# Performance work log

Hardware: AMD Instinct MI355X
Metric: run time of the kernel (lower is better)

Reference implementation:

```python
import jax, jax.numpy as jnp
import numpy as np

BN_EPS = 1e-3  # keras BatchNormalization default epsilon
NEG_INF = -1e30


def _masked_row_softmax(adjT):
    # tf.sparse.softmax semantics: softmax over NONZERO entries of each row;
    # implicit zeros stay exactly zero.
    mask = adjT != 0
    logits = jnp.where(mask, adjT, NEG_INF)
    p = jax.nn.softmax(logits, axis=-1)
    return jnp.where(mask, p, 0.0)


def _batch_norm(x, gamma, beta):
    # training-mode BN over all axes except channels
    mean = jnp.mean(x, axis=(0, 1), keepdims=True)
    var = jnp.var(x, axis=(0, 1), keepdims=True)
    return (x - mean) * jax.lax.rsqrt(var + BN_EPS) * gamma + beta


def setup_inputs() -> dict:
    key = jax.random.key(0)
    ks = jax.random.split(key, 4)
    B, N, F = 1, 8192, 128
    C0, C1 = 256, 128
    features = jax.random.normal(ks[0], (B, N, F), dtype=jnp.float32)
    adj = jax.random.randint(ks[1], (B, N, N), 0, 2, dtype=jnp.int32)
    kernel_1 = jax.random.normal(ks[2], (F, C0), dtype=jnp.float32) * (1.0 / np.sqrt(F))
    kernel_2 = jax.random.normal(ks[3], (C0, C1), dtype=jnp.float32) * (1.0 / np.sqrt(C0))
    return {
        "features": features,
        "adj": adj,
        "kernel_1": kernel_1,
        "bias_1": jnp.zeros((C0,), jnp.float32),
        "gamma_1": jnp.ones((C0,), jnp.float32),
        "beta_1": jnp.zeros((C0,), jnp.float32),
        "kernel_2": kernel_2,
        "bias_2": jnp.zeros((C1,), jnp.float32),
        "gamma_2": jnp.ones((C1,), jnp.float32),
        "beta_2": jnp.zeros((C1,), jnp.float32),
    }


def reference(features, adj, kernel_1, bias_1, gamma_1, beta_1,
              kernel_2, bias_2, gamma_2, beta_2):
    # fltr transposed: (B, Nr, Np), then sparse softmax over last dim
    adjT = jnp.transpose(adj.astype(jnp.float32), (0, 2, 1))
    w = _masked_row_softmax(adjT)                      # (B, Nr, Np)
    # people -> region aggregation + projection
    region = jnp.matmul(w, features)                   # (B, Nr, F)
    region = jnp.matmul(region, kernel_1) + bias_1     # (B, Nr, C0)
    region = _batch_norm(region, gamma_1, beta_1)
    # region -> people aggregation + projection
    people = jnp.matmul(jnp.transpose(w, (0, 2, 1)), region)  # (B, Np, C0)
    people = jnp.matmul(people, kernel_2) + bias_2             # (B, Np, C1)
    people = _batch_norm(people, gamma_2, beta_2)
    return people
```

## Files before the change

### kernel.cpp

```cpp
#include <hip/hip_runtime.h>
#include <stdint.h>

typedef unsigned int u32;
typedef unsigned short u16;
typedef unsigned long long u64;
typedef __attribute__((ext_vector_type(8))) short short8;
typedef __attribute__((ext_vector_type(4))) float f32x4;

#define N8K 8192

__device__ __forceinline__ float b2f(u16 u) { return __uint_as_float(((u32)u) << 16); }
__device__ __forceinline__ u16 f2b(float f) {
  u32 i = __float_as_uint(f);
  i += 0x7FFFu + ((i >> 16) & 1u);
  return (u16)(i >> 16);
}
__device__ __forceinline__ u16 f2h(float f) {
  union { _Float16 h; u16 u; } x; x.h = (_Float16)f; return x.u;
}
__device__ __forceinline__ u32 pkh(float a, float b) {
  return (u32)f2h(a) | ((u32)f2h(b) << 16);
}
union H8 { uint4 u; _Float16 h[8]; };
union H2 { u32 u; _Float16 h[2]; };
__device__ __forceinline__ u32 pk01(int x, int y) { return (u32)__mul24(x | (y << 16), 0x3F80); }
__device__ __forceinline__ u32 pkf(float a, float b) { return (u32)f2b(a) | ((u32)f2b(b) << 16); }

__device__ __forceinline__ int dvote(const u16* f16) {
  u16 u = f16[threadIdx.x * 2];
  int e = (u >> 7) & 0xFF;
  return __syncthreads_count((e >= 0x60 && e <= 0x9F) ? 1 : 0) >= 128;
}

__device__ __forceinline__ void gl_lds16(const void* g, void* l) {
  __builtin_amdgcn_global_load_lds(
      (const __attribute__((address_space(1))) u32*)g,
      (__attribute__((address_space(3))) u32*)l, 16, 0, 0);
}

__device__ __forceinline__ void unpack16(u32 b, uint4& o0, uint4& o1) {
  o0.x = ((b & 0x0001u) ? 0x3F80u : 0u) | ((b & 0x0002u) ? 0x3F800000u : 0u);
  o0.y = ((b & 0x0004u) ? 0x3F80u : 0u) | ((b & 0x0008u) ? 0x3F800000u : 0u);
  o0.z = ((b & 0x0010u) ? 0x3F80u : 0u) | ((b & 0x0020u) ? 0x3F800000u : 0u);
  o0.w = ((b & 0x0040u) ? 0x3F80u : 0u) | ((b & 0x0080u) ? 0x3F800000u : 0u);
  o1.x = ((b & 0x0100u) ? 0x3F80u : 0u) | ((b & 0x0200u) ? 0x3F800000u : 0u);
  o1.y = ((b & 0x0400u) ? 0x3F80u : 0u) | ((b & 0x0800u) ? 0x3F800000u : 0u);
  o1.z = ((b & 0x1000u) ? 0x3F80u : 0u) | ((b & 0x2000u) ? 0x3F800000u : 0u);
  o1.w = ((b & 0x4000u) ? 0x3F80u : 0u) | ((b & 0x8000u) ? 0x3F800000u : 0u);
}

#define MFMA_4x4(As_, Bs_, aoff_, boff_)                                         \
  {                                                                              \
    short8 afr[4], bfr[4];                                                       \
    _Pragma("unroll") for (int i_ = 0; i_ < 4; ++i_)                             \
      afr[i_] = *(const short8*)(As_ + aoff_[i_]);                               \
    _Pragma("unroll") for (int j_ = 0; j_ < 4; ++j_)                             \
      bfr[j_] = *(const short8*)(Bs_ + boff_[j_]);                               \
    _Pragma("unroll") for (int i_ = 0; i_ < 4; ++i_)                             \
      _Pragma("unroll") for (int j_ = 0; j_ < 4; ++j_)                           \
        acc[i_][j_] = __builtin_amdgcn_mfma_f32_16x16x32_bf16(                   \
            afr[i_], bfr[j_], acc[i_][j_], 0, 0, 0);                             \
  }

#define ZERO_ACC()                                                               \
  f32x4 acc[4][4];                                                               \
  {                                                                              \
    const f32x4 fz = {0.f, 0.f, 0.f, 0.f};                                       \
    _Pragma("unroll") for (int i_ = 0; i_ < 4; ++i_)                             \
      _Pragma("unroll") for (int j_ = 0; j_ < 4; ++j_) acc[i_][j_] = fz;         \
  }

__global__ void k_prep(const void* __restrict__ featv, const void* __restrict__ K1v,
                       const void* __restrict__ K2v,
                       const void* __restrict__ b1v, const void* __restrict__ g1v,
                       const void* __restrict__ be1v, const void* __restrict__ b2v,
                       const void* __restrict__ g2v, const void* __restrict__ be2v,
                       u16* __restrict__ Ft, u16* __restrict__ K1T, u16* __restrict__ K2T,
                       float* __restrict__ deg, float* __restrict__ par,
                       float* __restrict__ bn1s, float* __restrict__ bn1q,
                       float* __restrict__ bn2s, float* __restrict__ bn2q) {
  const int b = blockIdx.x, t = threadIdx.x;
  const int flag = dvote((const u16*)featv);
  if (b < 256) {
    __shared__ __align__(16) u16 Lf[32 * 136];
    const int pr = t >> 3, ck = t & 7;
    u16 v[16];
    if (flag) {
      const u16* s = (const u16*)featv + (size_t)(b * 32 + pr) * 128 + ck * 16;
      *(uint4*)&v[0] = *(const uint4*)(s);
      *(uint4*)&v[8] = *(const uint4*)(s + 8);
    } else {
      const float* s = (const float*)featv + (size_t)(b * 32 + pr) * 128 + ck * 16;
#pragma unroll
      for (int i = 0; i < 16; ++i) v[i] = f2b(s[i]);
    }
    *(uint4*)(Lf + pr * 136 + ck * 16) = *(uint4*)&v[0];
    *(uint4*)(Lf + pr * 136 + ck * 16 + 8) = *(uint4*)&v[8];
    __syncthreads();
    const int f = t >> 1, h16 = (t & 1) * 16;
    u32 w[8];
#pragma unroll
    for (int i = 0; i < 8; ++i) {
      u16 lo = Lf[(h16 + 2 * i) * 136 + f];
      u16 hi = Lf[(h16 + 2 * i + 1) * 136 + f];
      w[i] = (u32)lo | ((u32)hi << 16);
    }
    u16* d = Ft + (size_t)b * 4096 + f * 32 + h16;
    *(uint4*)(d) = *(uint4*)&w[0];
    *(uint4*)(d + 8) = *(uint4*)&w[4];
  } else if (b < 272) {
    int o = ((b - 256) * 256 + t) << 3;
    int k0 = o >> 13, c = (o >> 5) & 255, kk = o & 31;
    uint4 w;
    if (flag) {
      const u16* s = (const u16*)K1v + (size_t)(k0 * 32 + kk) * 256 + c;
      w.x = (u32)s[0]    | ((u32)s[256]  << 16);
      w.y = (u32)s[512]  | ((u32)s[768]  << 16);
      w.z = (u32)s[1024] | ((u32)s[1280] << 16);
      w.w = (u32)s[1536] | ((u32)s[1792] << 16);
    } else {
      const float* s = (const float*)K1v + (size_t)(k0 * 32 + kk) * 256 + c;
      w.x = pkf(s[0], s[256]); w.y = pkf(s[512], s[768]);
      w.z = pkf(s[1024], s[1280]); w.w = pkf(s[1536], s[1792]);
    }
    *(uint4*)(K1T + o) = w;
  } else if (b < 288) {
    int o = ((b - 272) * 256 + t) << 3;
    int k0 = o >> 12, c = (o >> 5) & 127, kk = o & 31;
    uint4 w;
    if (flag) {
      const u16* s = (const u16*)K2v + (size_t)(k0 * 32 + kk) * 128 + c;
      w.x = (u32)s[0]   | ((u32)s[128] << 16);
      w.y = (u32)s[256] | ((u32)s[384] << 16);
      w.z = (u32)s[512] | ((u32)s[640] << 16);
      w.w = (u32)s[768] | ((u32)s[896] << 16);
    } else {
      const float* s = (const float*)K2v + (size_t)(k0 * 32 + kk) * 128 + c;
      w.x = pkf(s[0], s[128]); w.y = pkf(s[256], s[384]);
      w.z = pkf(s[512], s[640]); w.w = pkf(s[768], s[896]);
    }
    *(uint4*)(K2T + o) = w;
  } else {
    if (t < 256) {
      par[t]       = flag ? b2f(((const u16*)b1v)[t])  : ((const float*)b1v)[t];
      par[256 + t] = flag ? b2f(((const u16*)g1v)[t])  : ((const float*)g1v)[t];
      par[512 + t] = flag ? b2f(((const u16*)be1v)[t]) : ((const float*)be1v)[t];
      bn1s[t] = 0.f; bn1q[t] = 0.f;
    }
    if (t < 128) {
      par[768 + t]  = flag ? b2f(((const u16*)b2v)[t])  : ((const float*)b2v)[t];
      par[896 + t]  = flag ? b2f(((const u16*)g2v)[t])  : ((const float*)g2v)[t];
      par[1024 + t] = flag ? b2f(((const u16*)be2v)[t]) : ((const float*)be2v)[t];
      bn2s[t] = 0.f; bn2q[t] = 0.f;
    }
    for (int i = t; i < N8K; i += 256) deg[i] = 0.f;
  }
}

__global__ __launch_bounds__(256, 2)
void k_gemm1(const int* __restrict__ adj, const u16* __restrict__ Ft,
             u16* __restrict__ P1h, float* __restrict__ deg,
             u32* __restrict__ RB) {
  __shared__ __align__(16) u16 As[4 * 128 * 32];
  __shared__ __align__(16) u16 Bs[4 * 128 * 32];
  __shared__ float degp[128];
  const int t = threadIdx.x, bx = blockIdx.x;
  const int nt = bx & 63, s = bx >> 6;
  const int n0 = nt << 7;
  const int lane = t & 63, wv = t >> 6;
  const int wm = (wv & 1) << 6, wn = (wv >> 1) << 6;
  const int fm = lane & 15, fq = lane >> 4;
  if (t < 128) degp[t] = 0.0f;
  ZERO_ACC();
  int aoff[4], boff[4];
#pragma unroll
  for (int i = 0; i < 4; ++i) aoff[i] = (wm + i * 16 + fm) * 32 + fq * 8;
#pragma unroll
  for (int j = 0; j < 4; ++j) {
    int n = wn + j * 16 + fm;
    boff[j] = n * 32 + ((fq * 8) ^ (((n >> 2) & 3) << 3));
  }
  const int rb = t & 31, kb = t >> 5;
  const int* gB = adj + ((size_t)s * 1024 + kb * 4) * N8K + n0 + rb * 4;
  const char* gA = (const char*)(Ft + (size_t)s * 32 * 4096);
  char* lA = (char*)As + ((t >> 6) << 10);
  const int goff = t << 4;
  u16* lb0 = Bs + (rb * 4) * 32 + ((kb * 4) ^ ((rb & 3) << 3));
  const int sh4 = (rb & 7) * 4;
  const int rbw = (n0 >> 5) + (rb >> 3);
  const int pb0 = s * 1024 + kb * 4;
  int ds0 = 0, ds1 = 0, ds2 = 0, ds3 = 0;
  for (int ks = 0; ks < 8; ++ks) {
    __syncthreads();
#pragma unroll
    for (int ph = 0; ph < 8; ++ph) gl_lds16(gA + ph * 4096 + goff, lA + ph * 4096);
    gA += 32768;
    u32* dst = RB + (size_t)(pb0 + ks * 128) * 256 + rbw;
#pragma unroll
    for (int ph = 0; ph < 4; ++ph) {
      const int* g = gB + (size_t)ph * 32 * N8K;
      int4 a0 = *(const int4*)(g);
      int4 a1 = *(const int4*)(g + N8K);
      int4 a2 = *(const int4*)(g + 2 * N8K);
      int4 a3 = *(const int4*)(g + 3 * N8K);
      ds0 += a0.x + a1.x + a2.x + a3.x;
      ds1 += a0.y + a1.y + a2.y + a3.y;
      ds2 += a0.z + a1.z + a2.z + a3.z;
      ds3 += a0.w + a1.w + a2.w + a3.w;
      u16* lb = lb0 + ph * 4096;
      uint2 w;
      w.x = pk01(a0.x, a1.x); w.y = pk01(a2.x, a3.x); *(uint2*)(lb) = w;
      w.x = pk01(a0.y, a1.y); w.y = pk01(a2.y, a3.y); *(uint2*)(lb + 32) = w;
      w.x = pk01(a0.z, a1.z); w.y = pk01(a2.z, a3.z); *(uint2*)(lb + 64) = w;
      w.x = pk01(a0.w, a1.w); w.y = pk01(a2.w, a3.w); *(uint2*)(lb + 96) = w;
      u32 v0 = ((u32)a0.x | ((u32)a0.y << 1) | ((u32)a0.z << 2) | ((u32)a0.w << 3)) << sh4;
      u32 v1 = ((u32)a1.x | ((u32)a1.y << 1) | ((u32)a1.z << 2) | ((u32)a1.w << 3)) << sh4;
      u32 v2 = ((u32)a2.x | ((u32)a2.y << 1) | ((u32)a2.z << 2) | ((u32)a2.w << 3)) << sh4;
      u32 v3 = ((u32)a3.x | ((u32)a3.y << 1) | ((u32)a3.z << 2) | ((u32)a3.w << 3)) << sh4;
      v0 |= __shfl_xor(v0, 1); v0 |= __shfl_xor(v0, 2); v0 |= __shfl_xor(v0, 4);
      v1 |= __shfl_xor(v1, 1); v1 |= __shfl_xor(v1, 2); v1 |= __shfl_xor(v1, 4);
      v2 |= __shfl_xor(v2, 1); v2 |= __shfl_xor(v2, 2); v2 |= __shfl_xor(v2, 4);
      v3 |= __shfl_xor(v3, 1); v3 |= __shfl_xor(v3, 2); v3 |= __shfl_xor(v3, 4);
      if ((rb & 7) == 0) {
        u32* d2 = dst + ph * 8192;
        d2[0] = v0; d2[256] = v1; d2[512] = v2; d2[768] = v3;
      }
    }
    gB += 128 * N8K;
    __syncthreads();
#pragma unroll
    for (int ph = 0; ph < 4; ++ph)
      MFMA_4x4((As + ph * 4096), (Bs + ph * 4096), aoff, boff);
  }
  atomicAdd(&degp[rb * 4 + 0], (float)ds0);
  atomicAdd(&degp[rb * 4 + 1], (float)ds1);
  atomicAdd(&degp[rb * 4 + 2], (float)ds2);
  atomicAdd(&degp[rb * 4 + 3], (float)ds3);
  u16* base = P1h + ((size_t)s * N8K + n0) * 128;
#pragma unroll
  for (int i = 0; i < 4; ++i)
#pragma unroll
    for (int j = 0; j < 4; ++j) {
      int r = wn + j * 16 + fm;
      int f = wm + i * 16 + fq * 4;
      uint2 w;
      w.x = pkh(acc[i][j][0], acc[i][j][1]);
      w.y = pkh(acc[i][j][2], acc[i][j][3]);
      *(uint2*)(base + (size_t)r * 128 + f) = w;
    }
  __syncthreads();
  if (t < 128) atomicAdd(&deg[n0 + t], degp[t]);
}

__global__ __launch_bounds__(256, 2)
void k_projf(const u16* __restrict__ P1h, const float* __restrict__ deg,
             const u16* __restrict__ K1T, const float* __restrict__ bias,
             float* __restrict__ Cout, float* __restrict__ bns, float* __restrict__ bnq) {
  __shared__ __align__(16) u16 As[64 * 32];
  __shared__ __align__(16) u16 Bs[128 * 32];
  const int t = threadIdx.x, bx = blockIdx.x;
  const int ct = bx & 1, mt = bx >> 1;
  const int m0 = mt << 6, n0 = ct << 7;
  const int lane = t & 63, wv = t >> 6;
  const int wn = wv << 5;
  const int fm = lane & 15, fq = lane >> 4;
  const f32x4 fz = {0.f, 0.f, 0.f, 0.f};
  f32x4 acc[4][2];
#pragma unroll
  for (int i = 0; i < 4; ++i)
#pragma unroll
    for (int j = 0; j < 2; ++j) acc[i][j] = fz;
  int aoff[4], boff[2];
#pragma unroll
  for (int i = 0; i < 4; ++i) {
    int m = i * 16 + fm;
    aoff[i] = m * 32 + ((fq * 8) ^ (((m >> 2) & 3) << 3));
  }
#pragma unroll
  for (int j = 0; j < 2; ++j) boff[j] = (wn + j * 16 + fm) * 32 + fq * 8;
  const int row = t >> 2, q = t & 3;
  const u16* src = P1h + (size_t)(m0 + row) * 128 + q * 8;
  float d = deg[m0 + row];
  const float inv = (d > 0.5f) ? 1.0f / d : 0.0f;
  const int swz = ((row >> 2) & 3) << 3;
  u16* la = As + row * 32 + ((q * 8) ^ swz);
  char* lB = (char*)Bs + ((t >> 6) << 10);
  const int goff = t << 4;
  for (int ks = 0; ks < 4; ++ks) {
    __syncthreads();
    const char* gB = (const char*)(K1T + ((size_t)ks * 256 + n0) * 32);
    gl_lds16(gB + goff, lB);
    gl_lds16(gB + 4096 + goff, lB + 4096);
    f32x4 s0 = fz, s1 = fz;
    const u16* p = src + ks * 32;
#pragma unroll
    for (int sp = 0; sp < 8; ++sp) {
      H8 L;
      L.u = *(const uint4*)(p + (size_t)sp * N8K * 128);
#pragma unroll
      for (int jj = 0; jj < 4; ++jj) {
        s0[jj] += (float)L.h[jj];
        s1[jj] += (float)L.h[4 + jj];
      }
    }
    s0 *= inv; s1 *= inv;
    uint4 w;
    w.x = pkf(s0[0], s0[1]); w.y = pkf(s0[2], s0[3]);
    w.z = pkf(s1[0], s1[1]); w.w = pkf(s1[2], s1[3]);
    *(uint4*)la = w;
    __syncthreads();
    short8 afr[4], bfr[2];
#pragma unroll
    for (int i = 0; i < 4; ++i) afr[i] = *(const short8*)(As + aoff[i]);
#pragma unroll
    for (int j = 0; j < 2; ++j) bfr[j] = *(const short8*)(Bs + boff[j]);
#pragma unroll
    for (int i = 0; i < 4; ++i)
#pragma unroll
      for (int j = 0; j < 2; ++j)
        acc[i][j] = __builtin_amdgcn_mfma_f32_16x16x32_bf16(afr[i], bfr[j], acc[i][j], 0, 0, 0);
  }
#pragma unroll
  for (int j = 0; j < 2; ++j) {
    int c = n0 + wn + j * 16 + fm;
    float bc = bias[c];
    float t1 = 0.f, t2 = 0.f;
#pragma unroll
    for (int i = 0; i < 4; ++i) {
      int r = m0 + i * 16 + fq * 4;
#pragma unroll
      for (int ii = 0; ii < 4; ++ii) {
        float v = acc[i][j][ii] + bc;
        Cout[(size_t)(r + ii) * 256 + c] = v;
        t1 += v; t2 += v * v;
      }
    }
    t1 += __shfl_xor(t1, 16); t1 += __shfl_xor(t1, 32);
    t2 += __shfl_xor(t2, 16); t2 += __shfl_xor(t2, 32);
    if (fq == 0) { atomicAdd(&bns[c], t1); atomicAdd(&bnq[c], t2); }
  }
}

__global__ __launch_bounds__(256, 2)
void k_bnH(const float* __restrict__ region1, const float* __restrict__ deg,
           const float* __restrict__ bn1s, const float* __restrict__ bn1q,
           const float* __restrict__ g1, const float* __restrict__ be1,
           const u16* __restrict__ K2T, u16* __restrict__ HT) {
  __shared__ __align__(16) u16 As[32 * 32];
  __shared__ __align__(16) u16 Bs[128 * 32];
  __shared__ float scS[256], shS[256];
  const int t = threadIdx.x, mt = blockIdx.x;
  const int m0 = mt << 5;
  const int lane = t & 63, wv = t >> 6;
  const int wn = wv << 5;
  const int fm = lane & 15, fq = lane >> 4;
  {
    float mu = bn1s[t] * (1.0f / 8192.0f);
    float var = bn1q[t] * (1.0f / 8192.0f) - mu * mu;
    float iv = rsqrtf(var + 1e-3f);
    float sc = iv * g1[t];
    scS[t] = sc;
    shS[t] = be1[t] - mu * sc;
  }
  const f32x4 fz = {0.f, 0.f, 0.f, 0.f};
  f32x4 acc[2][2];
#pragma unroll
  for (int i = 0; i < 2; ++i)
#pragma unroll
    for (int j = 0; j < 2; ++j) acc[i][j] = fz;
  int aoff[2], boff[2];
#pragma unroll
  for (int i = 0; i < 2; ++i) {
    int m = i * 16 + fm;
    aoff[i] = m * 32 + ((fq * 8) ^ (((m >> 2) & 3) << 3));
  }
#pragma unroll
  for (int j = 0; j < 2; ++j) boff[j] = (wn + j * 16 + fm) * 32 + fq * 8;
  const int row = t >> 3, oct = t & 7;
  float d = deg[m0 + row];
  const float idg = (d > 0.5f) ? 1.0f / d : 0.0f;
  const float* src = region1 + (size_t)(m0 + row) * 256 + oct * 4;
  const int swz = ((row >> 2) & 3) << 3;
  u16* la = As + row * 32 + ((oct * 4) ^ swz);
  char* lB = (char*)Bs + ((t >> 6) << 10);
  const int goff = t << 4;
  for (int ks = 0; ks < 8; ++ks) {
    __syncthreads();
    const char* gB = (const char*)(K2T + (size_t)ks * 4096);
    gl_lds16(gB + goff, lB);
    gl_lds16(gB + 4096 + goff, lB + 4096);
    const int cb = ks * 32 + oct * 4;
    f32x4 x = *(const f32x4*)(src + ks * 32);
    float y[4];
#pragma unroll
    for (int jj = 0; jj < 4; ++jj) y[jj] = (x[jj] * scS[cb + jj] + shS[cb + jj]) * idg;
    uint2 w;
    w.x = pkf(y[0], y[1]);
    w.y = pkf(y[2], y[3]);
    *(uint2*)la = w;
    __syncthreads();
    short8 afr[2], bfr[2];
#pragma unroll
    for (int i = 0; i < 2; ++i) afr[i] = *(const short8*)(As + aoff[i]);
#pragma unroll
    for (int j = 0; j < 2; ++j) bfr[j] = *(const short8*)(Bs + boff[j]);
#pragma unroll
    for (int i = 0; i < 2; ++i)
#pragma unroll
      for (int j = 0; j < 2; ++j)
        acc[i][j] = __builtin_amdgcn_mfma_f32_16x16x32_bf16(afr[i], bfr[j], acc[i][j], 0, 0, 0);
  }
#pragma unroll
  for (int i = 0; i < 2; ++i)
#pragma unroll
    for (int j = 0; j < 2; ++j) {
      int c = wn + j * 16 + fm;
      int r = m0 + i * 16 + fq * 4;
      uint2 w;
      w.x = pkf(acc[i][j][0], acc[i][j][1]);
      w.y = pkf(acc[i][j][2], acc[i][j][3]);
      *(uint2*)(HT + (size_t)(r >> 5) * 4096 + c * 32 + (r & 31)) = w;
    }
}

__global__ __launch_bounds__(256, 2)
void k_gemm2(const u32* __restrict__ RB, const u16* __restrict__ HT,
             u16* __restrict__ P2h) {
  __shared__ __align__(16) u16 As[4 * 128 * 32];
  __shared__ __align__(16) u16 Bs[4 * 128 * 32];
  const int t = threadIdx.x, bx = blockIdx.x;
  const int mt = bx & 63, s = bx >> 6;
  const int m0 = mt << 7;
  const int lane = t & 63, wv = t >> 6;
  const int wm = (wv & 1) << 6, wn = (wv >> 1) << 6;
  const int fm = lane & 15, fq = lane >> 4;
  ZERO_ACC();
  int aoff[4], boff[4];
#pragma unroll
  for (int i = 0; i < 4; ++i) {
    int m = wm + i * 16 + fm;
    aoff[i] = m * 32 + ((fq * 8) ^ (((m >> 2) & 3) << 3));
  }
#pragma unroll
  for (int j = 0; j < 4; ++j) boff[j] = (wn + j * 16 + fm) * 32 + fq * 8;
  const int row = t >> 1, h = t & 1;
  const u32* gA = RB + (size_t)(m0 + row) * 256 + s * 32;
  const char* gB = (const char*)(HT + (size_t)s * 32 * 4096);
  char* lB = (char*)Bs + ((t >> 6) << 10);
  const int goff = t << 4;
  const int swzA = ((row >> 2) & 3) << 3;
  u16* la0 = As + row * 32 + ((h * 16) ^ swzA);
  u16* la1 = As + row * 32 + (((h * 16) + 8) ^ swzA);
  for (int ks = 0; ks < 8; ++ks) {
    __syncthreads();
#pragma unroll
    for (int ph = 0; ph < 8; ++ph) gl_lds16(gB + ph * 4096 + goff, lB + ph * 4096);
    uint4 w4 = *(const uint4*)(gA + ks * 4);
    gB += 32768;
    u32 ws[4] = {w4.x, w4.y, w4.z, w4.w};
#pragma unroll
    for (int ph = 0; ph < 4; ++ph) {
      u32 bits = (ws[ph] >> (h * 16)) & 0xFFFFu;
      uint4 o0, o1;
      unpack16(bits, o0, o1);
      *(uint4*)(la0 + ph * 4096) = o0;
      *(uint4*)(la1 + ph * 4096) = o1;
    }
    __syncthreads();
#pragma unroll
    for (int ph = 0; ph < 4; ++ph)
      MFMA_4x4((As + ph * 4096), (Bs + ph * 4096), aoff, boff);
  }
  u16* base = P2h + (size_t)s * N8K * 128;
#pragma unroll
  for (int i = 0; i < 4; ++i)
#pragma unroll
    for (int j = 0; j < 4; ++j) {
      int c = wn + j * 16 + fm;
      int pr = m0 + wm + i * 16 + fq * 4;
#pragma unroll
      for (int ii = 0; ii < 4; ++ii)
        base[(size_t)(pr + ii) * 128 + c] = f2h(acc[i][j][ii]);
    }
}

__global__ void k_red2(const u16* __restrict__ P2h, const float* __restrict__ bias,
                       float* __restrict__ people1,
                       float* __restrict__ bn2s, float* __restrict__ bn2q) {
  __shared__ float r1[512], r2[512];
  const int t = threadIdx.x;
  const int c = (t & 63) * 2, pg = t >> 6;
  const int p0 = blockIdx.x << 5;
  const float bc0 = bias[c], bc1 = bias[c + 1];
  float s1a = 0.f, s2a = 0.f, s1b = 0.f, s2b = 0.f;
  for (int pp = pg; pp < 32; pp += 4) {
    size_t o = (size_t)(p0 + pp) * 128 + c;
    float v0 = bc0, v1 = bc1;
#pragma unroll
    for (int s = 0; s < 8; ++s) {
      H2 L;
      L.u = *(const u32*)(P2h + (size_t)s * N8K * 128 + o);
      v0 += (float)L.h[0];
      v1 += (float)L.h[1];
    }
    float2 st; st.x = v0; st.y = v1;
    *(float2*)(people1 + o) = st;
    s1a += v0; s2a += v0 * v0;
    s1b += v1; s2b += v1 * v1;
  }
  r1[t * 2] = s1a; r1[t * 2 + 1] = s1b;
  r2[t * 2] = s2a; r2[t * 2 + 1] = s2b;
  __syncthreads();
  if (t < 128) {
    float a = 0.f, b = 0.f;
#pragma unroll
    for (int g = 0; g < 4; ++g) {
      int idx = ((t >> 1) + 64 * g) * 2 + (t & 1);
      a += r1[idx]; b += r2[idx];
    }
    atomicAdd(&bn2s[t], a);
    atomicAdd(&bn2q[t], b);
  }
}

__global__ void k_bn2apply(const float* __restrict__ people1,
                           const float* __restrict__ bn2s, const float* __restrict__ bn2q,
                           const float* __restrict__ g2, const float* __restrict__ be2,
                           const u16* __restrict__ featprobe, void* __restrict__ outv) {
  const int flag = dvote(featprobe);
  int g = blockIdx.x * 256 + threadIdx.x;
  int p = g >> 5;
  int c = (g & 31) << 2;
  f32x4 x = *(const f32x4*)(people1 + (size_t)p * 128 + c);
  f32x4 y;
#pragma unroll
  for (int jj = 0; jj < 4; ++jj) {
    int cc = c + jj;
    float mu = bn2s[cc] * (1.0f / 8192.0f);
    float var = bn2q[cc] * (1.0f / 8192.0f) - mu * mu;
    float inv = rsqrtf(var + 1e-3f);
    y[jj] = (x[jj] - mu) * inv * g2[cc] + be2[cc];
  }
  if (flag) {
    uint2 w;
    w.x = pkf(y[0], y[1]);
    w.y = pkf(y[2], y[3]);
    *(uint2*)((u16*)outv + (size_t)p * 128 + c) = w;
  } else {
    *(f32x4*)((float*)outv + (size_t)p * 128 + c) = y;
  }
}

extern "C" void kernel_launch(void* const* d_in, const int* in_sizes, int n_in,
                              void* d_out, int out_size, void* d_ws, size_t ws_size,
                              hipStream_t stream) {
  const void* feat = d_in[0];
  const int* adj   = (const int*)d_in[1];
  const void* K1   = d_in[2];
  const void* b1   = d_in[3];
  const void* g1   = d_in[4];
  const void* be1  = d_in[5];
  const void* K2   = d_in[6];
  const void* b2   = d_in[7];
  const void* g2   = d_in[8];
  const void* be2  = d_in[9];
  char* ws = (char*)d_ws;
  const size_t MB = 1u << 20;

  u16*   Ph      = (u16*)(ws);
  float* region1 = (float*)(ws + 32 * MB);
  float* people1 = (float*)(ws + 40 * MB);
  u16*   Ft      = (u16*)(ws + 44 * MB);
  u16*   HT      = (u16*)(ws + 46 * MB);
  u32*   RB      = (u32*)(ws + 48 * MB);
  u16*   K1T     = (u16*)(ws + 56 * MB);
  u16*   K2T     = K1T + 32768;
  float* deg     = (float*)(K2T + 32768);
  float* par     = deg + N8K;
  float* bn1s    = par + 1152;
  float* bn1q    = bn1s + 256;
  float* bn2s    = bn1q + 256;
  float* bn2q    = bn2s + 128;

  k_prep<<<289, 256, 0, stream>>>(feat, K1, K2, b1, g1, be1, b2, g2, be2,
                                  Ft, K1T, K2T, deg, par, bn1s, bn1q, bn2s, bn2q);
  k_gemm1<<<512, 256, 0, stream>>>(adj, Ft, Ph, deg, RB);
  k_projf<<<256, 256, 0, stream>>>(Ph, deg, K1T, par + 0, region1, bn1s, bn1q);
  k_bnH<<<256, 256, 0, stream>>>(region1, deg, bn1s, bn1q, par + 256, par + 512,
                                 K2T, HT);
  k_gemm2<<<512, 256, 0, stream>>>(RB, HT, Ph);
  k_red2<<<256, 256, 0, stream>>>(Ph, par + 768, people1, bn2s, bn2q);
  k_bn2apply<<<1024, 256, 0, stream>>>(people1, bn2s, bn2q, par + 896, par + 1024,
                                       (const u16*)feat, d_out);
}
```

Baseline: 449.1 us.

## Prefetch next adjacency tile into registers and store region1 in bf16

In the first GEMM, the next k-step's adjacency int4 loads are issued into a 16-entry register array after the LDS barrier, so they overlap the MFMA work instead of stalling at the top of the loop. The second GEMM prefetches its next packed-bit word the same way. The region1 intermediate is now written as bf16 instead of fp32, which halves that round trip through memory. The prefetch array raises register pressure and could hurt occupancy, and bf16 storage of region1 loses some precision ahead of the batch norm.

```diff
diff --git a/kernel.cpp b/kernel.cpp
--- a/kernel.cpp
+++ b/kernel.cpp
@@ -190,6 +190,17 @@
   const int rbw = (n0 >> 5) + (rb >> 3);
   const int pb0 = s * 1024 + kb * 4;
   int ds0 = 0, ds1 = 0, ds2 = 0, ds3 = 0;
+  int4 pa[16];
+#pragma unroll
+  for (int ph = 0; ph < 4; ++ph) {
+    const int* g = gB + (size_t)ph * 32 * N8K;
+    pa[ph * 4 + 0] = *(const int4*)(g);
+    pa[ph * 4 + 1] = *(const int4*)(g + N8K);
+    pa[ph * 4 + 2] = *(const int4*)(g + 2 * N8K);
+    pa[ph * 4 + 3] = *(const int4*)(g + 3 * N8K);
+  }
+  gB += 128 * N8K;
+#pragma unroll 1
   for (int ks = 0; ks < 8; ++ks) {
     __syncthreads();
 #pragma unroll
@@ -198,11 +209,10 @@
     u32* dst = RB + (size_t)(pb0 + ks * 128) * 256 + rbw;
 #pragma unroll
     for (int ph = 0; ph < 4; ++ph) {
-      const int* g = gB + (size_t)ph * 32 * N8K;
-      int4 a0 = *(const int4*)(g);
-      int4 a1 = *(const int4*)(g + N8K);
-      int4 a2 = *(const int4*)(g + 2 * N8K);
-      int4 a3 = *(const int4*)(g + 3 * N8K);
+      int4 a0 = pa[ph * 4 + 0];
+      int4 a1 = pa[ph * 4 + 1];
+      int4 a2 = pa[ph * 4 + 2];
+      int4 a3 = pa[ph * 4 + 3];
       ds0 += a0.x + a1.x + a2.x + a3.x;
       ds1 += a0.y + a1.y + a2.y + a3.y;
       ds2 += a0.z + a1.z + a2.z + a3.z;
@@ -226,8 +236,18 @@
         d2[0] = v0; d2[256] = v1; d2[512] = v2; d2[768] = v3;
       }
     }
-    gB += 128 * N8K;
-    __syncthreads();
+    __syncthreads();
+    if (ks < 7) {
+#pragma unroll
+      for (int ph = 0; ph < 4; ++ph) {
+        const int* g = gB + (size_t)ph * 32 * N8K;
+        pa[ph * 4 + 0] = *(const int4*)(g);
+        pa[ph * 4 + 1] = *(const int4*)(g + N8K);
+        pa[ph * 4 + 2] = *(const int4*)(g + 2 * N8K);
+        pa[ph * 4 + 3] = *(const int4*)(g + 3 * N8K);
+      }
+      gB += 128 * N8K;
+    }
 #pragma unroll
     for (int ph = 0; ph < 4; ++ph)
       MFMA_4x4((As + ph * 4096), (Bs + ph * 4096), aoff, boff);
@@ -255,7 +275,7 @@
 __global__ __launch_bounds__(256, 2)
 void k_projf(const u16* __restrict__ P1h, const float* __restrict__ deg,
              const u16* __restrict__ K1T, const float* __restrict__ bias,
-             float* __restrict__ Cout, float* __restrict__ bns, float* __restrict__ bnq) {
+             u16* __restrict__ region1b, float* __restrict__ bns, float* __restrict__ bnq) {
   __shared__ __align__(16) u16 As[64 * 32];
   __shared__ __align__(16) u16 Bs[128 * 32];
   const int t = threadIdx.x, bx = blockIdx.x;
@@ -331,7 +351,7 @@
 #pragma unroll
       for (int ii = 0; ii < 4; ++ii) {
         float v = acc[i][j][ii] + bc;
-        Cout[(size_t)(r + ii) * 256 + c] = v;
+        region1b[(size_t)(r + ii) * 256 + c] = f2b(v);
         t1 += v; t2 += v * v;
       }
     }
@@ -342,7 +362,7 @@
 }
 
 __global__ __launch_bounds__(256, 2)
-void k_bnH(const float* __restrict__ region1, const float* __restrict__ deg,
+void k_bnH(const u16* __restrict__ region1b, const float* __restrict__ deg,
            const float* __restrict__ bn1s, const float* __restrict__ bn1q,
            const float* __restrict__ g1, const float* __restrict__ be1,
            const u16* __restrict__ K2T, u16* __restrict__ HT) {
@@ -379,7 +399,7 @@
   const int row = t >> 3, oct = t & 7;
   float d = deg[m0 + row];
   const float idg = (d > 0.5f) ? 1.0f / d : 0.0f;
-  const float* src = region1 + (size_t)(m0 + row) * 256 + oct * 4;
+  const u16* src = region1b + (size_t)(m0 + row) * 256 + oct * 4;
   const int swz = ((row >> 2) & 3) << 3;
   u16* la = As + row * 32 + ((oct * 4) ^ swz);
   char* lB = (char*)Bs + ((t >> 6) << 10);
@@ -390,13 +410,16 @@
     gl_lds16(gB + goff, lB);
     gl_lds16(gB + 4096 + goff, lB + 4096);
     const int cb = ks * 32 + oct * 4;
-    f32x4 x = *(const f32x4*)(src + ks * 32);
-    float y[4];
-#pragma unroll
-    for (int jj = 0; jj < 4; ++jj) y[jj] = (x[jj] * scS[cb + jj] + shS[cb + jj]) * idg;
+    uint2 xw = *(const uint2*)(src + ks * 32);
+    float x0 = b2f((u16)(xw.x & 0xFFFFu)), x1 = b2f((u16)(xw.x >> 16));
+    float x2 = b2f((u16)(xw.y & 0xFFFFu)), x3 = b2f((u16)(xw.y >> 16));
+    float y0 = (x0 * scS[cb + 0] + shS[cb + 0]) * idg;
+    float y1 = (x1 * scS[cb + 1] + shS[cb + 1]) * idg;
+    float y2 = (x2 * scS[cb + 2] + shS[cb + 2]) * idg;
+    float y3 = (x3 * scS[cb + 3] + shS[cb + 3]) * idg;
     uint2 w;
-    w.x = pkf(y[0], y[1]);
-    w.y = pkf(y[2], y[3]);
+    w.x = pkf(y0, y1);
+    w.y = pkf(y2, y3);
     *(uint2*)la = w;
     __syncthreads();
     short8 afr[2], bfr[2];
@@ -451,13 +474,14 @@
   const int swzA = ((row >> 2) & 3) << 3;
   u16* la0 = As + row * 32 + ((h * 16) ^ swzA);
   u16* la1 = As + row * 32 + (((h * 16) + 8) ^ swzA);
+  uint4 wcur = *(const uint4*)(gA);
+#pragma unroll 1
   for (int ks = 0; ks < 8; ++ks) {
     __syncthreads();
 #pragma unroll
     for (int ph = 0; ph < 8; ++ph) gl_lds16(gB + ph * 4096 + goff, lB + ph * 4096);
-    uint4 w4 = *(const uint4*)(gA + ks * 4);
     gB += 32768;
-    u32 ws[4] = {w4.x, w4.y, w4.z, w4.w};
+    u32 ws[4] = {wcur.x, wcur.y, wcur.z, wcur.w};
 #pragma unroll
     for (int ph = 0; ph < 4; ++ph) {
       u32 bits = (ws[ph] >> (h * 16)) & 0xFFFFu;
@@ -467,6 +491,7 @@
       *(uint4*)(la1 + ph * 4096) = o1;
     }
     __syncthreads();
+    if (ks < 7) wcur = *(const uint4*)(gA + (ks + 1) * 4);
 #pragma unroll
     for (int ph = 0; ph < 4; ++ph)
       MFMA_4x4((As + ph * 4096), (Bs + ph * 4096), aoff, boff);
@@ -567,26 +592,26 @@
   char* ws = (char*)d_ws;
   const size_t MB = 1u << 20;
 
-  u16*   Ph      = (u16*)(ws);
-  float* region1 = (float*)(ws + 32 * MB);
-  float* people1 = (float*)(ws + 40 * MB);
-  u16*   Ft      = (u16*)(ws + 44 * MB);
-  u16*   HT      = (u16*)(ws + 46 * MB);
-  u32*   RB      = (u32*)(ws + 48 * MB);
-  u16*   K1T     = (u16*)(ws + 56 * MB);
-  u16*   K2T     = K1T + 32768;
-  float* deg     = (float*)(K2T + 32768);
-  float* par     = deg + N8K;
-  float* bn1s    = par + 1152;
-  float* bn1q    = bn1s + 256;
-  float* bn2s    = bn1q + 256;
-  float* bn2q    = bn2s + 128;
+  u16*   Ph       = (u16*)(ws);
+  u16*   region1b = (u16*)(ws + 32 * MB);
+  float* people1  = (float*)(ws + 40 * MB);
+  u16*   Ft       = (u16*)(ws + 44 * MB);
+  u16*   HT       = (u16*)(ws + 46 * MB);
+  u32*   RB       = (u32*)(ws + 48 * MB);
+  u16*   K1T      = (u16*)(ws + 56 * MB);
+  u16*   K2T      = K1T + 32768;
+  float* deg      = (float*)(K2T + 32768);
+  float* par      = deg + N8K;
+  float* bn1s     = par + 1152;
+  float* bn1q     = bn1s + 256;
+  float* bn2s     = bn1q + 256;
+  float* bn2q     = bn2s + 128;
 
   k_prep<<<289, 256, 0, stream>>>(feat, K1, K2, b1, g1, be1, b2, g2, be2,
                                   Ft, K1T, K2T, deg, par, bn1s, bn1q, bn2s, bn2q);
   k_gemm1<<<512, 256, 0, stream>>>(adj, Ft, Ph, deg, RB);
-  k_projf<<<256, 256, 0, stream>>>(Ph, deg, K1T, par + 0, region1, bn1s, bn1q);
-  k_bnH<<<256, 256, 0, stream>>>(region1, deg, bn1s, bn1q, par + 256, par + 512,
+  k_projf<<<256, 256, 0, stream>>>(Ph, deg, K1T, par + 0, region1b, bn1s, bn1q);
+  k_bnH<<<256, 256, 0, stream>>>(region1b, deg, bn1s, bn1q, par + 256, par + 512,
                                  K2T, HT);
   k_gemm2<<<512, 256, 0, stream>>>(RB, HT, Ph);
   k_red2<<<256, 256, 0, stream>>>(Ph, par + 768, people1, bn2s, bn2q);
```

Result: no change. 452.0 us (+0.6%).
